# Performance work log

Hardware: AMD Instinct MI355X
Metric: run time of the kernel (lower is better)

The kernel has to match this reference:

```python
import jax, jax.numpy as jnp
import numpy as np

H = 64
VOCAB = 64
THRESH_SCALE = 0.4
LN_EPS = 1e-5
NORM_EPS = 1e-12


def setup_inputs() -> dict:
    key = jax.random.key(0)
    ks = jax.random.split(key, 16)
    B, L = 64, 1024
    s = 1.0 / np.sqrt(H)
    inp = {
        "seq": jax.random.randint(ks[0], (B, L), 0, VOCAB),
        "embed_W": jax.random.normal(ks[1], (VOCAB, H), jnp.float32),
        "ff_W1": jax.random.normal(ks[2], (H, 2 * H), jnp.float32) * s,
        "ff_b1": jnp.zeros((2 * H,), jnp.float32),
        "ff_W2": jax.random.normal(ks[3], (2 * H, H), jnp.float32) * s,
        "ff_b2": jnp.zeros((H,), jnp.float32),
        "ln_g": jnp.ones((H,), jnp.float32),
        "ln_b": jnp.zeros((H,), jnp.float32),
        "kp_W": jax.random.normal(ks[4], (H, H), jnp.float32) * s,
        "vp_W": jax.random.normal(ks[5], (H, H), jnp.float32) * s,
        "qp_W": jax.random.normal(ks[6], (H, H), jnp.float32) * s,
        "rp_W": jax.random.normal(ks[7], (H, H), jnp.float32) * s,
        "rp_b": jnp.zeros((H,), jnp.float32),
        "out_W": jax.random.normal(ks[8], (H, VOCAB), jnp.float32) * s,
        "out_b": jnp.zeros((VOCAB,), jnp.float32),
    }
    return inp


def _forward(seq, embed_W, ff_W1, ff_b1, ff_W2, ff_b2, ln_g, ln_b,
             kp_W, vp_W, qp_W, rp_W, rp_b, out_W, out_b):
    h = embed_W[seq]                                    # [B, L, H]
    ff = jnp.maximum(h @ ff_W1 + ff_b1, 0.0) @ ff_W2 + ff_b2
    x = h + ff
    mu = x.mean(-1, keepdims=True)
    var = ((x - mu) ** 2).mean(-1, keepdims=True)       # biased var (torch LayerNorm)
    hn = (x - mu) / jnp.sqrt(var + LN_EPS) * ln_g + ln_b
    B, L, _ = hn.shape

    # Precompute all per-step keys/values, then scan the fast-weight update.
    k_all = hn[:, :-1] @ kp_W                           # [B, L-1, H]
    v_all = hn[:, :-1] @ vp_W                           # [B, L-1, H]
    kn_all = k_all / jnp.maximum(
        jnp.linalg.norm(k_all, axis=-1, keepdims=True), NORM_EPS)

    def step(M, kv):
        kn, v = kv                                      # each [B, H]
        vp = jnp.einsum('bij,bj->bi', M, kn)            # read M along k
        err = jnp.linalg.norm(v - vp, axis=-1)          # [B]
        gate = jnp.where(err > THRESH_SCALE * jnp.linalg.norm(v, axis=-1),
                         1.0, 0.0)                      # hard energy gate
        M = M + gate[:, None, None] * jnp.einsum('bi,bj->bij', v - vp, kn)
        return M, None

    M0 = jnp.zeros((B, H, H), dtype=hn.dtype)
    M, _ = jax.lax.scan(step, M0,
                        (kn_all.transpose(1, 0, 2), v_all.transpose(1, 0, 2)))

    q = hn[:, -1] @ qp_W                                # [B, H]
    r = jnp.einsum('bij,bj->bi', M, q) @ rp_W + rp_b
    return r @ out_W + out_b                            # [B, VOCAB]


def reference(seq, embed_W, ff_W1, ff_b1, ff_W2, ff_b2, ln_g, ln_b,
              kp_W, vp_W, qp_W, rp_W, rp_b, out_W, out_b):
    return _forward(seq, embed_W, ff_W1, ff_b1, ff_W2, ff_b2, ln_g, ln_b,
                    kp_W, vp_W, qp_W, rp_W, rp_b, out_W, out_b)
```

## Files before the change

### kernel.cpp

```cpp
#include <hip/hip_runtime.h>
#include <hip/hip_bf16.h>
#include <math.h>

#define BB 64
#define LL 1024
#define HH 64

typedef float v4f __attribute__((ext_vector_type(4)));
#define F4 __builtin_elementwise_fma

__global__ __launch_bounds__(256, 1)
void token_kernel(const int* __restrict__ seq,
                  const float* __restrict__ embed_W,
                  const float* __restrict__ ff_W1, const float* __restrict__ ff_b1,
                  const float* __restrict__ ff_W2, const float* __restrict__ ff_b2,
                  const float* __restrict__ ln_g, const float* __restrict__ ln_b,
                  const float* __restrict__ kp_W, const float* __restrict__ vp_W,
                  const float* __restrict__ qp_W,
                  float* __restrict__ knv, float* __restrict__ vthr,
                  float* __restrict__ qbuf)
{
    __shared__ __align__(16) float h_s[32][64];
    __shared__ __align__(16) float t1_s[32][128];
    __shared__ __align__(16) float hn_s[32][64];

    const int tid  = threadIdx.x;
    const int tok0 = blockIdx.x * 32;

#pragma unroll
    for (int k = 0; k < 8; ++k) {
        int e   = k * 256 + tid;
        int tok = e >> 6, i = e & 63;
        int s   = seq[tok0 + tok];
        h_s[tok][i] = embed_W[s * 64 + i];
    }
    __syncthreads();

    {
        const int j = tid & 127;
        const int g = tid >> 7;
        float w1c[64];
#pragma unroll
        for (int ii = 0; ii < 64; ++ii) w1c[ii] = ff_W1[ii * 128 + j];
        const float b1j = ff_b1[j];
#pragma unroll
        for (int tk = 0; tk < 16; ++tk) {
            const int tok = g * 16 + tk;
            const float4* h4 = (const float4*)h_s[tok];
            float a0 = b1j, a1 = 0.f, a2 = 0.f, a3 = 0.f;
#pragma unroll
            for (int w = 0; w < 16; ++w) {
                float4 hv = h4[w];
                a0 = fmaf(hv.x, w1c[4*w+0], a0);
                a1 = fmaf(hv.y, w1c[4*w+1], a1);
                a2 = fmaf(hv.z, w1c[4*w+2], a2);
                a3 = fmaf(hv.w, w1c[4*w+3], a3);
            }
            t1_s[tok][j] = fmaxf((a0 + a1) + (a2 + a3), 0.f);
        }
    }
    __syncthreads();

    {
        const int i  = tid & 63;
        const int w4 = tid >> 6;
        const float b2i = ff_b2[i];
        const float gi  = ln_g[i];
        const float bi  = ln_b[i];
        float accf[8];
#pragma unroll
        for (int tk = 0; tk < 8; ++tk) accf[tk] = b2i;
#pragma unroll
        for (int h = 0; h < 2; ++h) {
            float w2c[64];
#pragma unroll
            for (int jj = 0; jj < 64; ++jj) w2c[jj] = ff_W2[(h*64 + jj) * 64 + i];
#pragma unroll
            for (int tk = 0; tk < 8; ++tk) {
                const int tok = w4 * 8 + tk;
                const float4* t4 = (const float4*)&t1_s[tok][h*64];
                float a0 = 0.f, a1 = 0.f, a2 = 0.f, a3 = 0.f;
#pragma unroll
                for (int w = 0; w < 16; ++w) {
                    float4 tv = t4[w];
                    a0 = fmaf(tv.x, w2c[4*w+0], a0);
                    a1 = fmaf(tv.y, w2c[4*w+1], a1);
                    a2 = fmaf(tv.z, w2c[4*w+2], a2);
                    a3 = fmaf(tv.w, w2c[4*w+3], a3);
                }
                accf[tk] += (a0 + a1) + (a2 + a3);
            }
        }
#pragma unroll
        for (int tk = 0; tk < 8; ++tk) {
            const int tok = w4 * 8 + tk;
            float x = h_s[tok][i] + accf[tk];
            float s = x;
#pragma unroll
            for (int m = 32; m > 0; m >>= 1) s += __shfl_xor(s, m);
            float mu = s * (1.f / 64.f);
            float d  = x - mu;
            float s2 = d * d;
#pragma unroll
            for (int m = 32; m > 0; m >>= 1) s2 += __shfl_xor(s2, m);
            float var = s2 * (1.f / 64.f);
            hn_s[tok][i] = d / sqrtf(var + 1e-5f) * gi + bi;
        }
    }
    __syncthreads();

    {
        const int i  = tid & 63;
        const int w4 = tid >> 6;
        float kc[64], vc[64];
#pragma unroll
        for (int ii = 0; ii < 64; ++ii) {
            kc[ii] = kp_W[ii * 64 + i];
            vc[ii] = vp_W[ii * 64 + i];
        }
#pragma unroll
        for (int tk = 0; tk < 8; ++tk) {
            const int tok = w4 * 8 + tk;
            const int tg  = tok0 + tok;
            const int b   = tg >> 10;
            const int t   = tg & 1023;
            const float4* hn4 = (const float4*)hn_s[tok];
            if (t < 1023) {
                float ka0=0.f,ka1=0.f,ka2=0.f,ka3=0.f;
                float va0=0.f,va1=0.f,va2=0.f,va3=0.f;
#pragma unroll
                for (int w = 0; w < 16; ++w) {
                    float4 hv = hn4[w];
                    ka0 = fmaf(hv.x, kc[4*w+0], ka0);
                    ka1 = fmaf(hv.y, kc[4*w+1], ka1);
                    ka2 = fmaf(hv.z, kc[4*w+2], ka2);
                    ka3 = fmaf(hv.w, kc[4*w+3], ka3);
                    va0 = fmaf(hv.x, vc[4*w+0], va0);
                    va1 = fmaf(hv.y, vc[4*w+1], va1);
                    va2 = fmaf(hv.z, vc[4*w+2], va2);
                    va3 = fmaf(hv.w, vc[4*w+3], va3);
                }
                float ka = (ka0 + ka1) + (ka2 + ka3);
                float va = (va0 + va1) + (va2 + va3);
                float kn2 = ka * ka, vn2 = va * va;
#pragma unroll
                for (int m = 32; m > 0; m >>= 1) {
                    kn2 += __shfl_xor(kn2, m);
                    vn2 += __shfl_xor(vn2, m);
                }
                float knorm = fmaxf(sqrtf(kn2), 1e-12f);
                size_t row = ((size_t)b * 1024 + t) * 128;
                knv[row + i]      = ka / knorm;
                knv[row + 64 + i] = va;
                if (i == 0) vthr[b * 1024 + t] = 0.16f * vn2;
            } else {
                float qa0=0.f,qa1=0.f,qa2=0.f,qa3=0.f;
#pragma unroll
                for (int w = 0; w < 16; ++w) {
                    float4 hv = hn4[w];
                    qa0 = fmaf(hv.x, qp_W[(4*w+0)*64 + i], qa0);
                    qa1 = fmaf(hv.y, qp_W[(4*w+1)*64 + i], qa1);
                    qa2 = fmaf(hv.z, qp_W[(4*w+2)*64 + i], qa2);
                    qa3 = fmaf(hv.w, qp_W[(4*w+3)*64 + i], qa3);
                }
                qbuf[b * 64 + i] = (qa0 + qa1) + (qa2 + qa3);
            }
        }
    }
}


template<int CTRL>
__device__ __forceinline__ float dppadd(float x) {
    int y = __builtin_amdgcn_update_dpp(0, __float_as_int(x), CTRL, 0xF, 0xF, true);
    return x + __int_as_float(y);
}

__device__ __forceinline__ float bcast63(float x) {
    return __int_as_float(__builtin_amdgcn_readlane(__float_as_int(x), 63));
}

__device__ __forceinline__ float wave_sum64(float x) {
    x = dppadd<0x111>(x); x = dppadd<0x112>(x);
    x = dppadd<0x114>(x); x = dppadd<0x118>(x);
    x = dppadd<0x142>(x); x = dppadd<0x143>(x);
    return bcast63(x);
}

__device__ __forceinline__ void wsum8(float& a, float& b, float& c, float& d,
                                      float& e, float& f, float& g, float& h) {
#define LVL(C) a=dppadd<C>(a); b=dppadd<C>(b); c=dppadd<C>(c); d=dppadd<C>(d); \
               e=dppadd<C>(e); f=dppadd<C>(f); g=dppadd<C>(g); h=dppadd<C>(h);
    LVL(0x111) LVL(0x112) LVL(0x114) LVL(0x118) LVL(0x142) LVL(0x143)
#undef LVL
    a=bcast63(a); b=bcast63(b); c=bcast63(c); d=bcast63(d);
    e=bcast63(e); f=bcast63(f); g=bcast63(g); h=bcast63(h);
}

#define LOADK4(P, ROW) do { \
    const float* r_ = (ROW) + (wid << 4); \
    P##0 = *(const v4f*)(r_ + 0);  P##1 = *(const v4f*)(r_ + 4); \
    P##2 = *(const v4f*)(r_ + 8);  P##3 = *(const v4f*)(r_ + 12); \
} while (0)

#define UPD4(P, G) do { \
    v4f gv_ = {G, G, G, G}; \
    m0 = F4(gv_, P##0, m0); m1 = F4(gv_, P##1, m1); \
    m2 = F4(gv_, P##2, m2); m3 = F4(gv_, P##3, m3); \
} while (0)

#define CHUNK2L(P0_, P1_, ROW2, ROW3, TH2P, TH3P, PAR) do { \
    float2 p0_ = ((const float2*)pex[(PAR)^1][0])[lane]; \
    float2 p1_ = ((const float2*)pex[(PAR)^1][1])[lane]; \
    float2 p2_ = ((const float2*)pex[(PAR)^1][2])[lane]; \
    float2 p3_ = ((const float2*)pex[(PAR)^1][3])[lane]; \
    UPD4(P0_, gdp); \
    UPD4(P1_, gdq); \
    LOADK4(P0_, ROW2); \
    LOADK4(P1_, ROW3); \
    float knl2_ = (ROW2)[lane]; \
    float knl3_ = (ROW3)[lane]; \
    float vv2_  = (ROW2)[64 + lane]; \
    float vv3_  = (ROW3)[64 + lane]; \
    float th2_  = *(TH2P); \
    float th3_  = *(TH3P); \
    float base0_ = (p0_.x + p1_.x) + (p2_.x + p3_.x); \
    float base1_ = (p0_.y + p1_.y) + (p2_.y + p3_.y); \
    float vp0_ = fmaf(Gb0, gdq, fmaf(Ga0, gdp, base0_)); \
    float vp1_ = fmaf(Gb1, gdq, fmaf(Ga1, gdp, base1_)); \
    float d00_ = vv0 - vp0_; \
    float d01_ = vv1 - vp1_; \
    float x0_ = d00_ * d00_, x1_ = d00_ * d01_, x2_ = d01_ * d01_; \
    float y0_ = knl0 * knl2_, y1_ = knl1 * knl2_; \
    float y2_ = knl0 * knl3_, y3_ = knl1 * knl3_, y4_ = knl2_ * knl3_; \
    wsum8(x0_, x1_, x2_, y0_, y1_, y2_, y3_, y4_); \
    bool g0_ = x0_ > th0; \
    float corr_ = fmaf(2.f * c01, x1_, -(c01 * c01) * x0_); \
    float e1_ = g0_ ? (x2_ - corr_) : x2_; \
    bool g1_ = e1_ > th1; \
    float gd0_ = g0_ ? d00_ : 0.f; \
    float d1_  = fmaf(-c01, gd0_, d01_); \
    gdp = gd0_; \
    gdq = g1_ ? d1_ : 0.f; \
    v4f q_ = F4(m0, P0_##0, F4(m1, P0_##1, F4(m2, P0_##2, m3 * P0_##3))); \
    float own0_ = (q_.x + q_.y) + (q_.z + q_.w); \
    v4f r_ = F4(m0, P1_##0, F4(m1, P1_##1, F4(m2, P1_##2, m3 * P1_##3))); \
    float own1_ = (r_.x + r_.y) + (r_.z + r_.w); \
    ((float2*)pex[PAR][wid])[lane] = make_float2(own0_, own1_); \
    knl0 = knl2_; knl1 = knl3_; vv0 = vv2_; vv1 = vv3_; th0 = th2_; th1 = th3_; \
    Ga0 = y0_; Gb0 = y1_; Ga1 = y2_; Gb1 = y3_; c01 = y4_; \
    asm volatile("s_waitcnt lgkmcnt(0)\n\ts_barrier" ::: "memory"); \
} while (0)

#define BUF8L(CB, NB, TP) \
    CHUNK2L(U,V,(CB)+2*128, (CB)+3*128, (TP)+2, (TP)+3, 0); \
    CHUNK2L(S,T,(CB)+4*128, (CB)+5*128, (TP)+4, (TP)+5, 1); \
    CHUNK2L(U,V,(CB)+6*128, (CB)+7*128, (TP)+6, (TP)+7, 0); \
    CHUNK2L(S,T,(CB)+8*128, (CB)+9*128, (TP)+8, (TP)+9, 1); \
    CHUNK2L(U,V,(CB)+10*128,(CB)+11*128,(TP)+10,(TP)+11,0); \
    CHUNK2L(S,T,(CB)+12*128,(CB)+13*128,(TP)+12,(TP)+13,1); \
    CHUNK2L(U,V,(CB)+14*128,(CB)+15*128,(TP)+14,(TP)+15,0); \
    CHUNK2L(S,T,(NB)+0*128, (NB)+1*128, (TP)+16,(TP)+17,1);

__device__ __forceinline__ void gl2lds_1k(const float* g, float* l, int lane) {
    __builtin_amdgcn_global_load_lds(
        (const __attribute__((address_space(1))) void*)(g + lane * 4),
        (__attribute__((address_space(3))) void*)l, 16, 0, 0);
}

__device__ __forceinline__ void prefetch_quarter(const float* g, float* l,
                                                 int lane, int wid) {
#pragma unroll
    for (int j = 0; j < 2; ++j)
        gl2lds_1k(g + wid * 512 + j * 256, l + wid * 512 + j * 256, lane);
}

__global__ __launch_bounds__(256, 1)
void scan_kernel(const float* __restrict__ knv,
                 const float* __restrict__ vthr,
                 const float* __restrict__ qbuf,
                 const float* __restrict__ rp_W, const float* __restrict__ rp_b,
                 const float* __restrict__ out_W, const float* __restrict__ out_b,
                 float* __restrict__ out)
{
    const int b    = blockIdx.x;
    const int tid  = threadIdx.x;
    const int lane = tid & 63;
    const int wid  = tid >> 6;
    const float* knvb = knv  + (size_t)b * 1024 * 128;
    const float* thrb = vthr + (size_t)b * 1024;

    __shared__ __align__(16) float thr_s[1040];
    __shared__ __align__(16) float buf[3 * 2048];
    __shared__ __align__(16) float pex[2][4][128];
    __shared__ float sh[64];

    v4f m0={0,0,0,0}, m1={0,0,0,0}, m2={0,0,0,0}, m3={0,0,0,0};
    v4f S0,S1,S2,S3;
    v4f T0,T1,T2,T3;
    v4f U0,U1,U2,U3;
    v4f V0,V1,V2,V3;

    if (wid == 0) {
#pragma unroll
        for (int w = 0; w < 4; ++w) gl2lds_1k(thrb + w * 256, thr_s + w * 256, lane);
    }
    prefetch_quarter(knvb,        buf,        lane, wid);
    prefetch_quarter(knvb + 2048, buf + 2048, lane, wid);
    prefetch_quarter(knvb + 4096, buf + 4096, lane, wid);

    {
        float4 z4 = make_float4(0.f, 0.f, 0.f, 0.f);
        ((float4*)pex)[tid] = z4;
    }

    asm volatile("s_waitcnt vmcnt(2) lgkmcnt(0)\n\ts_barrier" ::: "memory");

    LOADK4(S, buf);
    LOADK4(T, buf + 128);
    {
        v4f z_ = {0.f, 0.f, 0.f, 0.f};
        U0=z_;U1=z_;U2=z_;U3=z_;
        V0=z_;V1=z_;V2=z_;V3=z_;
    }
    float knl0 = buf[lane];
    float knl1 = buf[128 + lane];
    float vv0  = buf[64 + lane];
    float vv1  = buf[192 + lane];
    float th0  = thr_s[0];
    float th1  = thr_s[1];
    float c01  = wave_sum64(knl0 * knl1);
    float Ga0 = 0.f, Gb0 = 0.f, Ga1 = 0.f, Gb1 = 0.f;
    float gdp = 0.f, gdq = 0.f;

#pragma unroll 1
    for (int c = 0; c < 62; ++c) {
        asm volatile("s_waitcnt vmcnt(2)" ::: "memory");
        const float* cb = buf + (c % 3) * 2048;
        const float* nb = buf + ((c + 1) % 3) * 2048;
        const float* tp = thr_s + c * 16;
        BUF8L(cb, nb, tp)
        if (c <= 60)
            prefetch_quarter(knvb + (size_t)(c + 3) * 2048,
                             buf + (c % 3) * 2048, lane, wid);
    }
    asm volatile("s_waitcnt vmcnt(0)" ::: "memory");
    asm volatile("s_barrier" ::: "memory");
    {
        const float* cb = buf + 2 * 2048;
        const float* nb = buf;
        const float* tp = thr_s + 62 * 16;
        BUF8L(cb, nb, tp)
    }
    {
        const float* cb = buf;
        const float* nb = buf + 2048;
        const float* tp = thr_s + 63 * 16;
        BUF8L(cb, nb, tp)
    }
    UPD4(U, gdp);

    {
        const v4f* qq = (const v4f*)(qbuf + b * 64);
        const int w4i = 4 * wid;
        v4f aq = F4(m0, qq[w4i+0], F4(m1, qq[w4i+1],
                 F4(m2, qq[w4i+2],  m3 * qq[w4i+3])));
        float vq_own = (aq.x + aq.y) + (aq.z + aq.w);
        pex[0][wid][lane] = vq_own;
        asm volatile("s_waitcnt lgkmcnt(0)\n\ts_barrier" ::: "memory");

        if (wid == 0) {
            float vq = (pex[0][0][lane] + pex[0][1][lane])
                     + (pex[0][2][lane] + pex[0][3][lane]);
            sh[lane] = vq;
            asm volatile("s_waitcnt lgkmcnt(0)" ::: "memory");
            float r = rp_b[lane];
#pragma unroll
            for (int ii = 0; ii < 64; ++ii) r = fmaf(sh[ii], rp_W[ii * 64 + lane], r);
            asm volatile("s_waitcnt lgkmcnt(0)" ::: "memory");
            sh[lane] = r;
            asm volatile("s_waitcnt lgkmcnt(0)" ::: "memory");
            float o = out_b[lane];
#pragma unroll
            for (int ii = 0; ii < 64; ++ii) o = fmaf(sh[ii], out_W[ii * 64 + lane], o);
            out[b * 64 + lane] = o;
        }
    }
}

extern "C" void kernel_launch(void* const* d_in, const int* in_sizes, int n_in,
                              void* d_out, int out_size, void* d_ws, size_t ws_size,
                              hipStream_t stream)
{
    const int*   seq   = (const int*)  d_in[0];
    const float* embed = (const float*)d_in[1];
    const float* ffW1  = (const float*)d_in[2];
    const float* ffb1  = (const float*)d_in[3];
    const float* ffW2  = (const float*)d_in[4];
    const float* ffb2  = (const float*)d_in[5];
    const float* lng   = (const float*)d_in[6];
    const float* lnb   = (const float*)d_in[7];
    const float* kpW   = (const float*)d_in[8];
    const float* vpW   = (const float*)d_in[9];
    const float* qpW   = (const float*)d_in[10];
    const float* rpW   = (const float*)d_in[11];
    const float* rpb   = (const float*)d_in[12];
    const float* outW  = (const float*)d_in[13];
    const float* outb  = (const float*)d_in[14];
    float* out = (float*)d_out;

    float* knv  = (float*)d_ws;
    float* vthr = knv  + (size_t)64 * 1024 * 128;
    float* qbuf = vthr + (size_t)64 * 1024;

    token_kernel<<<2048, 256, 0, stream>>>(seq, embed, ffW1, ffb1, ffW2, ffb2,
                                           lng, lnb, kpW, vpW, qpW,
                                           knv, vthr, qbuf);
    scan_kernel<<<64, 256, 0, stream>>>(knv, vthr, qbuf,
                                        rpW, rpb, outW, outb, out);
}
```

Baseline: 395.7 us.

## Interleave two batch scans per block to hide barrier and reduction latency

Each scan block now processes two batch rows, A and B, interleaved in the same instruction stream. The dependent latency chains (LDS exchange, barrier, wave reduction, gate logic) of one row can overlap with the other. The previous cross-step Gram-correction terms are dropped: the partial products are now exchanged after the update rather than before it. The grid is halved to 32 blocks, so parallelism across CUs drops while register pressure and per-block work roughly double.

```diff
diff --git a/kernel.cpp b/kernel.cpp
--- a/kernel.cpp
+++ b/kernel.cpp
@@ -203,64 +203,92 @@
     P##2 = *(const v4f*)(r_ + 8);  P##3 = *(const v4f*)(r_ + 12); \
 } while (0)
 
-#define UPD4(P, G) do { \
+#define UPD4M(M, P, G) do { \
     v4f gv_ = {G, G, G, G}; \
-    m0 = F4(gv_, P##0, m0); m1 = F4(gv_, P##1, m1); \
-    m2 = F4(gv_, P##2, m2); m3 = F4(gv_, P##3, m3); \
+    M##0 = F4(gv_, P##0, M##0); M##1 = F4(gv_, P##1, M##1); \
+    M##2 = F4(gv_, P##2, M##2); M##3 = F4(gv_, P##3, M##3); \
 } while (0)
 
-#define CHUNK2L(P0_, P1_, ROW2, ROW3, TH2P, TH3P, PAR) do { \
-    float2 p0_ = ((const float2*)pex[(PAR)^1][0])[lane]; \
-    float2 p1_ = ((const float2*)pex[(PAR)^1][1])[lane]; \
-    float2 p2_ = ((const float2*)pex[(PAR)^1][2])[lane]; \
-    float2 p3_ = ((const float2*)pex[(PAR)^1][3])[lane]; \
-    UPD4(P0_, gdp); \
-    UPD4(P1_, gdq); \
-    LOADK4(P0_, ROW2); \
-    LOADK4(P1_, ROW3); \
-    float knl2_ = (ROW2)[lane]; \
-    float knl3_ = (ROW3)[lane]; \
-    float vv2_  = (ROW2)[64 + lane]; \
-    float vv3_  = (ROW3)[64 + lane]; \
-    float th2_  = *(TH2P); \
-    float th3_  = *(TH3P); \
-    float base0_ = (p0_.x + p1_.x) + (p2_.x + p3_.x); \
-    float base1_ = (p0_.y + p1_.y) + (p2_.y + p3_.y); \
-    float vp0_ = fmaf(Gb0, gdq, fmaf(Ga0, gdp, base0_)); \
-    float vp1_ = fmaf(Gb1, gdq, fmaf(Ga1, gdp, base1_)); \
-    float d00_ = vv0 - vp0_; \
-    float d01_ = vv1 - vp1_; \
-    float x0_ = d00_ * d00_, x1_ = d00_ * d01_, x2_ = d01_ * d01_; \
-    float y0_ = knl0 * knl2_, y1_ = knl1 * knl2_; \
-    float y2_ = knl0 * knl3_, y3_ = knl1 * knl3_, y4_ = knl2_ * knl3_; \
-    wsum8(x0_, x1_, x2_, y0_, y1_, y2_, y3_, y4_); \
-    bool g0_ = x0_ > th0; \
-    float corr_ = fmaf(2.f * c01, x1_, -(c01 * c01) * x0_); \
-    float e1_ = g0_ ? (x2_ - corr_) : x2_; \
-    bool g1_ = e1_ > th1; \
-    float gd0_ = g0_ ? d00_ : 0.f; \
-    float d1_  = fmaf(-c01, gd0_, d01_); \
-    gdp = gd0_; \
-    gdq = g1_ ? d1_ : 0.f; \
-    v4f q_ = F4(m0, P0_##0, F4(m1, P0_##1, F4(m2, P0_##2, m3 * P0_##3))); \
-    float own0_ = (q_.x + q_.y) + (q_.z + q_.w); \
-    v4f r_ = F4(m0, P1_##0, F4(m1, P1_##1, F4(m2, P1_##2, m3 * P1_##3))); \
-    float own1_ = (r_.x + r_.y) + (r_.z + r_.w); \
-    ((float2*)pex[PAR][wid])[lane] = make_float2(own0_, own1_); \
-    knl0 = knl2_; knl1 = knl3_; vv0 = vv2_; vv1 = vv3_; th0 = th2_; th1 = th3_; \
-    Ga0 = y0_; Gb0 = y1_; Ga1 = y2_; Gb1 = y3_; c01 = y4_; \
+#define CHUNK2AB(UP, UQ, XR, XS, RA2, RA3, TPA2, TPA3, PAR) do { \
+    UPD4M(mA, UP##A, gdpA);  UPD4M(mB, UP##B, gdpB); \
+    UPD4M(mA, UQ##A, gdqA);  UPD4M(mB, UQ##B, gdqB); \
+    v4f qA_ = F4(mA0, XR##A0, F4(mA1, XR##A1, F4(mA2, XR##A2, mA3 * XR##A3))); \
+    float own0A_ = (qA_.x + qA_.y) + (qA_.z + qA_.w); \
+    v4f rA_ = F4(mA0, XS##A0, F4(mA1, XS##A1, F4(mA2, XS##A2, mA3 * XS##A3))); \
+    float own1A_ = (rA_.x + rA_.y) + (rA_.z + rA_.w); \
+    v4f qB_ = F4(mB0, XR##B0, F4(mB1, XR##B1, F4(mB2, XR##B2, mB3 * XR##B3))); \
+    float own0B_ = (qB_.x + qB_.y) + (qB_.z + qB_.w); \
+    v4f rB_ = F4(mB0, XS##B0, F4(mB1, XS##B1, F4(mB2, XS##B2, mB3 * XS##B3))); \
+    float own1B_ = (rB_.x + rB_.y) + (rB_.z + rB_.w); \
+    ((float2*)pexA[PAR][wid])[lane] = make_float2(own0A_, own1A_); \
+    ((float2*)pexB[PAR][wid])[lane] = make_float2(own0B_, own1B_); \
     asm volatile("s_waitcnt lgkmcnt(0)\n\ts_barrier" ::: "memory"); \
+    float2 p0A_ = ((const float2*)pexA[PAR][0])[lane]; \
+    float2 p1A_ = ((const float2*)pexA[PAR][1])[lane]; \
+    float2 p2A_ = ((const float2*)pexA[PAR][2])[lane]; \
+    float2 p3A_ = ((const float2*)pexA[PAR][3])[lane]; \
+    float2 p0B_ = ((const float2*)pexB[PAR][0])[lane]; \
+    float2 p1B_ = ((const float2*)pexB[PAR][1])[lane]; \
+    float2 p2B_ = ((const float2*)pexB[PAR][2])[lane]; \
+    float2 p3B_ = ((const float2*)pexB[PAR][3])[lane]; \
+    float knl2A_ = (RA2)[lane]; \
+    float knl3A_ = (RA3)[lane]; \
+    float vv2A_  = (RA2)[64 + lane]; \
+    float vv3A_  = (RA3)[64 + lane]; \
+    float knl2B_ = (RA2)[6144 + lane]; \
+    float knl3B_ = (RA3)[6144 + lane]; \
+    float vv2B_  = (RA2)[6144 + 64 + lane]; \
+    float vv3B_  = (RA3)[6144 + 64 + lane]; \
+    float th2A_  = *(TPA2); \
+    float th3A_  = *(TPA3); \
+    float th2B_  = *((TPA2) + 1024); \
+    float th3B_  = *((TPA3) + 1024); \
+    LOADK4(UP##A, RA2); \
+    LOADK4(UQ##A, RA3); \
+    LOADK4(UP##B, (RA2) + 6144); \
+    LOADK4(UQ##B, (RA3) + 6144); \
+    float base0A_ = (p0A_.x + p1A_.x) + (p2A_.x + p3A_.x); \
+    float base1A_ = (p0A_.y + p1A_.y) + (p2A_.y + p3A_.y); \
+    float base0B_ = (p0B_.x + p1B_.x) + (p2B_.x + p3B_.x); \
+    float base1B_ = (p0B_.y + p1B_.y) + (p2B_.y + p3B_.y); \
+    float d00A_ = vv0A - base0A_; \
+    float d01A_ = vv1A - base1A_; \
+    float d00B_ = vv0B - base0B_; \
+    float d01B_ = vv1B - base1B_; \
+    float x0A_ = d00A_ * d00A_, x1A_ = d00A_ * d01A_; \
+    float x2A_ = d01A_ * d01A_, x3A_ = knl2A_ * knl3A_; \
+    float x0B_ = d00B_ * d00B_, x1B_ = d00B_ * d01B_; \
+    float x2B_ = d01B_ * d01B_, x3B_ = knl2B_ * knl3B_; \
+    wsum8(x0A_, x1A_, x2A_, x3A_, x0B_, x1B_, x2B_, x3B_); \
+    bool g0A_ = x0A_ > th0A; \
+    float corrA_ = fmaf(2.f * c3A, x1A_, -(c3A * c3A) * x0A_); \
+    float e1A_ = g0A_ ? (x2A_ - corrA_) : x2A_; \
+    bool g1A_ = e1A_ > th1A; \
+    float gd0A_ = g0A_ ? d00A_ : 0.f; \
+    float d1A_  = fmaf(-c3A, gd0A_, d01A_); \
+    gdpA = gd0A_; \
+    gdqA = g1A_ ? d1A_ : 0.f; \
+    bool g0B_ = x0B_ > th0B; \
+    float corrB_ = fmaf(2.f * c3B, x1B_, -(c3B * c3B) * x0B_); \
+    float e1B_ = g0B_ ? (x2B_ - corrB_) : x2B_; \
+    bool g1B_ = e1B_ > th1B; \
+    float gd0B_ = g0B_ ? d00B_ : 0.f; \
+    float d1B_  = fmaf(-c3B, gd0B_, d01B_); \
+    gdpB = gd0B_; \
+    gdqB = g1B_ ? d1B_ : 0.f; \
+    vv0A = vv2A_; vv1A = vv3A_; th0A = th2A_; th1A = th3A_; c3A = x3A_; \
+    vv0B = vv2B_; vv1B = vv3B_; th0B = th2B_; th1B = th3B_; c3B = x3B_; \
 } while (0)
 
-#define BUF8L(CB, NB, TP) \
-    CHUNK2L(U,V,(CB)+2*128, (CB)+3*128, (TP)+2, (TP)+3, 0); \
-    CHUNK2L(S,T,(CB)+4*128, (CB)+5*128, (TP)+4, (TP)+5, 1); \
-    CHUNK2L(U,V,(CB)+6*128, (CB)+7*128, (TP)+6, (TP)+7, 0); \
-    CHUNK2L(S,T,(CB)+8*128, (CB)+9*128, (TP)+8, (TP)+9, 1); \
-    CHUNK2L(U,V,(CB)+10*128,(CB)+11*128,(TP)+10,(TP)+11,0); \
-    CHUNK2L(S,T,(CB)+12*128,(CB)+13*128,(TP)+12,(TP)+13,1); \
-    CHUNK2L(U,V,(CB)+14*128,(CB)+15*128,(TP)+14,(TP)+15,0); \
-    CHUNK2L(S,T,(NB)+0*128, (NB)+1*128, (TP)+16,(TP)+17,1);
+#define BUF8AB(CB, NB, TP) \
+    CHUNK2AB(U,V,S,T,(CB)+2*128, (CB)+3*128, (TP)+2, (TP)+3, 0); \
+    CHUNK2AB(S,T,U,V,(CB)+4*128, (CB)+5*128, (TP)+4, (TP)+5, 1); \
+    CHUNK2AB(U,V,S,T,(CB)+6*128, (CB)+7*128, (TP)+6, (TP)+7, 0); \
+    CHUNK2AB(S,T,U,V,(CB)+8*128, (CB)+9*128, (TP)+8, (TP)+9, 1); \
+    CHUNK2AB(U,V,S,T,(CB)+10*128,(CB)+11*128,(TP)+10,(TP)+11,0); \
+    CHUNK2AB(S,T,U,V,(CB)+12*128,(CB)+13*128,(TP)+12,(TP)+13,1); \
+    CHUNK2AB(U,V,S,T,(CB)+14*128,(CB)+15*128,(TP)+14,(TP)+15,0); \
+    CHUNK2AB(S,T,U,V,(NB)+0*128, (NB)+1*128, (TP)+16,(TP)+17,1);
 
 __device__ __forceinline__ void gl2lds_1k(const float* g, float* l, int lane) {
     __builtin_amdgcn_global_load_lds(
@@ -283,107 +311,139 @@
                  const float* __restrict__ out_W, const float* __restrict__ out_b,
                  float* __restrict__ out)
 {
-    const int b    = blockIdx.x;
+    const int p    = blockIdx.x;
+    const int bA   = 2 * p;
+    const int bB   = 2 * p + 1;
     const int tid  = threadIdx.x;
     const int lane = tid & 63;
     const int wid  = tid >> 6;
-    const float* knvb = knv  + (size_t)b * 1024 * 128;
-    const float* thrb = vthr + (size_t)b * 1024;
-
-    __shared__ __align__(16) float thr_s[1040];
-    __shared__ __align__(16) float buf[3 * 2048];
-    __shared__ __align__(16) float pex[2][4][128];
+    const float* knvbA = knv  + (size_t)bA * 1024 * 128;
+    const float* knvbB = knv  + (size_t)bB * 1024 * 128;
+    const float* thrbA = vthr + (size_t)bA * 1024;
+
+    __shared__ __align__(16) float bufAB[2 * 6144];
+    __shared__ __align__(16) float pexA[2][4][128];
+    __shared__ __align__(16) float pexB[2][4][128];
     __shared__ float sh[64];
-
-    v4f m0={0,0,0,0}, m1={0,0,0,0}, m2={0,0,0,0}, m3={0,0,0,0};
-    v4f S0,S1,S2,S3;
-    v4f T0,T1,T2,T3;
-    v4f U0,U1,U2,U3;
-    v4f V0,V1,V2,V3;
-
-    if (wid == 0) {
-#pragma unroll
-        for (int w = 0; w < 4; ++w) gl2lds_1k(thrb + w * 256, thr_s + w * 256, lane);
-    }
-    prefetch_quarter(knvb,        buf,        lane, wid);
-    prefetch_quarter(knvb + 2048, buf + 2048, lane, wid);
-    prefetch_quarter(knvb + 4096, buf + 4096, lane, wid);
+    float* bufA = bufAB;
+    float* bufB = bufAB + 6144;
+
+    v4f mA0={0,0,0,0}, mA1={0,0,0,0}, mA2={0,0,0,0}, mA3={0,0,0,0};
+    v4f mB0={0,0,0,0}, mB1={0,0,0,0}, mB2={0,0,0,0}, mB3={0,0,0,0};
+    v4f SA0,SA1,SA2,SA3, TA0,TA1,TA2,TA3, UA0,UA1,UA2,UA3, VA0,VA1,VA2,VA3;
+    v4f SB0,SB1,SB2,SB3, TB0,TB1,TB2,TB3, UB0,UB1,UB2,UB3, VB0,VB1,VB2,VB3;
+
+    prefetch_quarter(knvbA,        bufA,        lane, wid);
+    prefetch_quarter(knvbB,        bufB,        lane, wid);
+    prefetch_quarter(knvbA + 2048, bufA + 2048, lane, wid);
+    prefetch_quarter(knvbB + 2048, bufB + 2048, lane, wid);
+    prefetch_quarter(knvbA + 4096, bufA + 4096, lane, wid);
+    prefetch_quarter(knvbB + 4096, bufB + 4096, lane, wid);
 
     {
         float4 z4 = make_float4(0.f, 0.f, 0.f, 0.f);
-        ((float4*)pex)[tid] = z4;
-    }
-
-    asm volatile("s_waitcnt vmcnt(2) lgkmcnt(0)\n\ts_barrier" ::: "memory");
-
-    LOADK4(S, buf);
-    LOADK4(T, buf + 128);
+        ((float4*)pexA)[tid] = z4;
+        ((float4*)pexB)[tid] = z4;
+    }
+
+    asm volatile("s_waitcnt vmcnt(4) lgkmcnt(0)\n\ts_barrier" ::: "memory");
+
+    LOADK4(SA, bufA);
+    LOADK4(TA, bufA + 128);
+    LOADK4(SB, bufB);
+    LOADK4(TB, bufB + 128);
     {
         v4f z_ = {0.f, 0.f, 0.f, 0.f};
-        U0=z_;U1=z_;U2=z_;U3=z_;
-        V0=z_;V1=z_;V2=z_;V3=z_;
-    }
-    float knl0 = buf[lane];
-    float knl1 = buf[128 + lane];
-    float vv0  = buf[64 + lane];
-    float vv1  = buf[192 + lane];
-    float th0  = thr_s[0];
-    float th1  = thr_s[1];
-    float c01  = wave_sum64(knl0 * knl1);
-    float Ga0 = 0.f, Gb0 = 0.f, Ga1 = 0.f, Gb1 = 0.f;
-    float gdp = 0.f, gdq = 0.f;
+        UA0=z_;UA1=z_;UA2=z_;UA3=z_; VA0=z_;VA1=z_;VA2=z_;VA3=z_;
+        UB0=z_;UB1=z_;UB2=z_;UB3=z_; VB0=z_;VB1=z_;VB2=z_;VB3=z_;
+    }
+    float vv0A = bufA[64 + lane];
+    float vv1A = bufA[192 + lane];
+    float vv0B = bufB[64 + lane];
+    float vv1B = bufB[192 + lane];
+    float th0A = thrbA[0];
+    float th1A = thrbA[1];
+    float th0B = thrbA[1024];
+    float th1B = thrbA[1025];
+    float c3A  = wave_sum64(bufA[lane] * bufA[128 + lane]);
+    float c3B  = wave_sum64(bufB[lane] * bufB[128 + lane]);
+    float gdpA = 0.f, gdqA = 0.f, gdpB = 0.f, gdqB = 0.f;
 
 #pragma unroll 1
     for (int c = 0; c < 62; ++c) {
-        asm volatile("s_waitcnt vmcnt(2)" ::: "memory");
-        const float* cb = buf + (c % 3) * 2048;
-        const float* nb = buf + ((c + 1) % 3) * 2048;
-        const float* tp = thr_s + c * 16;
-        BUF8L(cb, nb, tp)
-        if (c <= 60)
-            prefetch_quarter(knvb + (size_t)(c + 3) * 2048,
-                             buf + (c % 3) * 2048, lane, wid);
+        asm volatile("s_waitcnt vmcnt(4)" ::: "memory");
+        const float* cb = bufA + (c % 3) * 2048;
+        const float* nb = bufA + ((c + 1) % 3) * 2048;
+        const float* tp = thrbA + c * 16;
+        BUF8AB(cb, nb, tp)
+        if (c <= 60) {
+            prefetch_quarter(knvbA + (size_t)(c + 3) * 2048,
+                             bufA + (c % 3) * 2048, lane, wid);
+            prefetch_quarter(knvbB + (size_t)(c + 3) * 2048,
+                             bufB + (c % 3) * 2048, lane, wid);
+        }
     }
     asm volatile("s_waitcnt vmcnt(0)" ::: "memory");
     asm volatile("s_barrier" ::: "memory");
     {
-        const float* cb = buf + 2 * 2048;
-        const float* nb = buf;
-        const float* tp = thr_s + 62 * 16;
-        BUF8L(cb, nb, tp)
-    }
-    {
-        const float* cb = buf;
-        const float* nb = buf + 2048;
-        const float* tp = thr_s + 63 * 16;
-        BUF8L(cb, nb, tp)
-    }
-    UPD4(U, gdp);
-
-    {
-        const v4f* qq = (const v4f*)(qbuf + b * 64);
+        const float* cb = bufA + 2 * 2048;
+        const float* nb = bufA;
+        const float* tp = thrbA + 62 * 16;
+        BUF8AB(cb, nb, tp)
+    }
+    {
+        const float* cb = bufA;
+        const float* nb = bufA + 2048;
+        const float* tp = thrbA + 63 * 16;
+        BUF8AB(cb, nb, tp)
+    }
+    UPD4M(mA, UA, gdpA);
+    UPD4M(mB, UB, gdpB);
+
+    {
+        const v4f* qqA = (const v4f*)(qbuf + bA * 64);
         const int w4i = 4 * wid;
-        v4f aq = F4(m0, qq[w4i+0], F4(m1, qq[w4i+1],
-                 F4(m2, qq[w4i+2],  m3 * qq[w4i+3])));
-        float vq_own = (aq.x + aq.y) + (aq.z + aq.w);
-        pex[0][wid][lane] = vq_own;
+        v4f aqA = F4(mA0, qqA[w4i+0], F4(mA1, qqA[w4i+1],
+                  F4(mA2, qqA[w4i+2],  mA3 * qqA[w4i+3])));
+        float vqA_own = (aqA.x + aqA.y) + (aqA.z + aqA.w);
+        const v4f* qqB = (const v4f*)(qbuf + bB * 64);
+        v4f aqB = F4(mB0, qqB[w4i+0], F4(mB1, qqB[w4i+1],
+                  F4(mB2, qqB[w4i+2],  mB3 * qqB[w4i+3])));
+        float vqB_own = (aqB.x + aqB.y) + (aqB.z + aqB.w);
+        pexA[0][wid][lane] = vqA_own;
+        pexB[0][wid][lane] = vqB_own;
         asm volatile("s_waitcnt lgkmcnt(0)\n\ts_barrier" ::: "memory");
 
         if (wid == 0) {
-            float vq = (pex[0][0][lane] + pex[0][1][lane])
-                     + (pex[0][2][lane] + pex[0][3][lane]);
-            sh[lane] = vq;
-            asm volatile("s_waitcnt lgkmcnt(0)" ::: "memory");
-            float r = rp_b[lane];
-#pragma unroll
-            for (int ii = 0; ii < 64; ++ii) r = fmaf(sh[ii], rp_W[ii * 64 + lane], r);
-            asm volatile("s_waitcnt lgkmcnt(0)" ::: "memory");
-            sh[lane] = r;
-            asm volatile("s_waitcnt lgkmcnt(0)" ::: "memory");
-            float o = out_b[lane];
-#pragma unroll
-            for (int ii = 0; ii < 64; ++ii) o = fmaf(sh[ii], out_W[ii * 64 + lane], o);
-            out[b * 64 + lane] = o;
+            float vqA = (pexA[0][0][lane] + pexA[0][1][lane])
+                      + (pexA[0][2][lane] + pexA[0][3][lane]);
+            sh[lane] = vqA;
+            asm volatile("s_waitcnt lgkmcnt(0)" ::: "memory");
+            float rA = rp_b[lane];
+#pragma unroll
+            for (int ii = 0; ii < 64; ++ii) rA = fmaf(sh[ii], rp_W[ii * 64 + lane], rA);
+            asm volatile("s_waitcnt lgkmcnt(0)" ::: "memory");
+            sh[lane] = rA;
+            asm volatile("s_waitcnt lgkmcnt(0)" ::: "memory");
+            float oA = out_b[lane];
+#pragma unroll
+            for (int ii = 0; ii < 64; ++ii) oA = fmaf(sh[ii], out_W[ii * 64 + lane], oA);
+            out[bA * 64 + lane] = oA;
+            asm volatile("s_waitcnt lgkmcnt(0)" ::: "memory");
+            float vqB = (pexB[0][0][lane] + pexB[0][1][lane])
+                      + (pexB[0][2][lane] + pexB[0][3][lane]);
+            sh[lane] = vqB;
+            asm volatile("s_waitcnt lgkmcnt(0)" ::: "memory");
+            float rB = rp_b[lane];
+#pragma unroll
+            for (int ii = 0; ii < 64; ++ii) rB = fmaf(sh[ii], rp_W[ii * 64 + lane], rB);
+            asm volatile("s_waitcnt lgkmcnt(0)" ::: "memory");
+            sh[lane] = rB;
+            asm volatile("s_waitcnt lgkmcnt(0)" ::: "memory");
+            float oB = out_b[lane];
+#pragma unroll
+            for (int ii = 0; ii < 64; ++ii) oB = fmaf(sh[ii], out_W[ii * 64 + lane], oB);
+            out[bB * 64 + lane] = oB;
         }
     }
 }
@@ -416,6 +476,6 @@
     token_kernel<<<2048, 256, 0, stream>>>(seq, embed, ffW1, ffb1, ffW2, ffb2,
                                            lng, lnb, kpW, vpW, qpW,
                                            knv, vthr, qbuf);
-    scan_kernel<<<64, 256, 0, stream>>>(knv, vthr, qbuf,
+    scan_kernel<<<32, 256, 0, stream>>>(knv, vthr, qbuf,
                                         rpW, rpb, outW, outb, out);
 }
```

Result: slower. 509.1 us (+28.7%).
